# Kernel tuning notes

Measured on AMD Instinct MI355X. Metric: run time of the kernel, lower is better.

Reference implementation:

```python
import jax, jax.numpy as jnp
import numpy as np

EPS = 1e-5
NEG = -1e9

def _ln(x, g, b):
    m = x.mean(-1, keepdims=True)
    v = ((x - m) ** 2).mean(-1, keepdims=True)
    return (x - m) / jnp.sqrt(v + EPS) * g + b

def setup_inputs() -> dict:
    key = jax.random.key(0)
    ks = jax.random.split(key, 32)
    B, N, D, F, L = 2, 512, 128, 512, 3
    s = 0.05
    rn = lambda k, sh, sc=s: jax.random.normal(k, sh, jnp.float32) * sc
    inp = {
        'rel_matrix': rn(ks[0], (B, N, N, 2), 1.0),
        'pre_w': rn(ks[1], (2, D)), 'pre_b': rn(ks[2], (D,)),
        'proj_w': rn(ks[3], (2 * D, D)), 'proj_b': rn(ks[4], (D,)),
        'out_w1': rn(ks[5], (D, D)),
        'bn_g': 1.0 + rn(ks[6], (D,)), 'bn_b': rn(ks[7], (D,)),
        'bn_m': rn(ks[8], (D,)),
        'bn_v': 0.5 + jax.random.uniform(ks[9], (D,), jnp.float32),
        'out_w2': rn(ks[10], (D, D)), 'out_b2': rn(ks[11], (D,)),
        'pe': rn(ks[12], (128, D)),
        'wq': rn(ks[13], (L, D, D)), 'bq': rn(ks[14], (L, D)),
        'wk': rn(ks[15], (L, D, D)), 'bk': rn(ks[16], (L, D)),
        'wv': rn(ks[17], (L, D, D)), 'bv': rn(ks[18], (L, D)),
        'wo': rn(ks[19], (L, D, D)), 'bo': rn(ks[20], (L, D)),
        'ln1g': jnp.ones((L, D), jnp.float32), 'ln1b': jnp.zeros((L, D), jnp.float32),
        'ln2g': jnp.ones((L, D), jnp.float32), 'ln2b': jnp.zeros((L, D), jnp.float32),
        'fw1': rn(ks[21], (L, D, F)), 'fb1': rn(ks[22], (L, F)),
        'fw2': rn(ks[23], (L, F, D)), 'fb2': rn(ks[24], (L, D)),
        'mask': jax.random.randint(ks[25], (B, N), 0, 2) > 0,
        'agent_id': jax.random.randint(ks[26], (B, N), 0, 128, dtype=jnp.int32),
    }
    return inp

def reference(rel_matrix, pre_w, pre_b, proj_w, proj_b, out_w1, bn_g, bn_b, bn_m, bn_v,
              out_w2, out_b2, pe, wq, bq, wk, bk, wv, bv, wo, bo,
              ln1g, ln1b, ln2g, ln2b, fw1, fb1, fw2, fb2, mask, agent_id):
    # --- pairwise relation chain (the headroom target) ---
    # symmetric pairwise validity mask (B,N,N)
    pm = (mask[:, None, :] & mask[:, :, None]).astype(rel_matrix.dtype)
    count = jnp.maximum(pm.sum(axis=2), 1.0)  # (B,N) valid-partner counts
    x = rel_matrix @ pre_w + pre_b            # (B,N,N,D) pre_proj Linear(2->128)
    pooled = jnp.einsum('bijd,bij->bid', x, pm) / count[..., None]  # masked mean over j
    x = jnp.concatenate([x, jnp.broadcast_to(pooled[:, :, None, :], x.shape)], axis=-1)
    x = x @ proj_w + proj_b                   # Linear(256->128)
    x = jnp.einsum('bijd,bij->bid', x, pm) / count[..., None]       # masked mean over j
    # out MLP: Linear(no bias) + BatchNorm1d(eval) + ReLU + Linear
    h = x @ out_w1
    h = (h - bn_m) / jnp.sqrt(bn_v + EPS) * bn_g + bn_b
    x = jax.nn.relu(h) @ out_w2 + out_b2
    x = x + pe[agent_id]                      # agent positional embedding
    # --- 3 post-norm single-head transformer layers (eval, dropout off) ---
    kbias = jnp.where(mask, 0.0, NEG)[:, None, :]  # key padding bias (B,1,N)
    scale = 1.0 / jnp.sqrt(jnp.asarray(x.shape[-1], x.dtype))
    for l in range(3):
        q = x @ wq[l] + bq[l]
        k = x @ wk[l] + bk[l]
        v = x @ wv[l] + bv[l]
        a = jax.nn.softmax(jnp.einsum('bid,bjd->bij', q, k) * scale + kbias, axis=-1)
        att = jnp.einsum('bij,bjd->bid', a, v) @ wo[l] + bo[l]
        x = _ln(x + att, ln1g[l], ln1b[l])
        ff = jax.nn.relu(x @ fw1[l] + fb1[l]) @ fw2[l] + fb2[l]
        x = _ln(x + ff, ln2g[l], ln2b[l])
    return x
```

## Files before the change

kernel.cpp:

```cpp
#include <hip/hip_runtime.h>
#include <hip/hip_bf16.h>

typedef unsigned short u16;
typedef unsigned int u32;
typedef unsigned char u8;
typedef __attribute__((ext_vector_type(8))) short bf16x8;
typedef __attribute__((ext_vector_type(4))) float f32x4;

#define DEV __device__ __forceinline__

DEV float bf2f(u16 u) { union { u32 i; float f; } c; c.i = ((u32)u) << 16; return c.f; }
DEV u16 f2bf(float f) {
  union { float f; u32 i; } c; c.f = f;
  u32 r = c.i + 0x7FFFu + ((c.i >> 16) & 1u);
  return (u16)(r >> 16);
}
DEV u32 pk2(float lo, float hi) { return (u32)f2bf(lo) | ((u32)f2bf(hi) << 16); }
DEV float rdsrc(const void* p, int e, int isb) {
  return isb ? bf2f(((const u16*)p)[e]) : ((const float*)p)[e];
}
DEV bf16x8 as_bf(uint4 v) { union { uint4 u; bf16x8 h; } c; c.u = v; return c.h; }

static constexpr int B = 2, N = 512, D = 128, F = 512;
static constexpr int NROW = B * N;
static constexpr float EPS = 1e-5f;
static constexpr float NEG = -1e9f;
static constexpr float SCALE = 0.08838834764831845f;

#define OFF_PRE_W   0
#define OFF_PRE_B   256
#define OFF_PROJ_B  33152
#define OFF_BN_G    49664
#define OFF_BN_B    49792
#define OFF_BN_M    49920
#define OFF_BN_V    50048
#define OFF_OUT_B2  66560
#define OFF_PE      66688
#define OFF_BQ      132224
#define OFF_BK      181760
#define OFF_BV      231296
#define OFF_BO      280832
#define OFF_LN1G    281216
#define OFF_LN1B    281600
#define OFF_LN2G    281984
#define OFF_LN2B    282368
#define OFF_FB1     479360
#define OFF_FB2     677504
#define W_TOTAL     677888

static constexpr int PB_PROJ = 0;
static constexpr int PB_OW1  = 8192;
static constexpr int PB_OW2  = 16384;
static constexpr int PB_L0   = 24576;
static constexpr int PB_LSTR = 98304;
static constexpr int PB_WO   = 24576;
static constexpr int PB_FW1  = 32768;
static constexpr int PB_FW2  = 65536;
static constexpr int PTOT    = 79872;

struct NEnt { const void* s; int off, n; };
struct PEnt { const void* s1; const void* s2; int o1, o2, dst, lgn, cum; };
struct PrepArgs { NEnt nrm[19]; PEnt pk[21]; };

template<int KT>
DEV f32x4 mmaKo(const uint4* __restrict__ aPk, const uint4* __restrict__ Bp,
                int ncol, int col, int lane, int kt0) {
  f32x4 acc = {0.f, 0.f, 0.f, 0.f};
  const int sub = lane >> 4;
  #pragma unroll
  for (int kt = 0; kt < KT; ++kt) {
    const int e8 = (kt0 + kt) * 4 + sub;
    acc = __builtin_amdgcn_mfma_f32_16x16x32_bf16(
        as_bf(aPk[e8 * 16 + (lane & 15)]),
        as_bf(Bp[(size_t)e8 * ncol + col]),
        acc, 0, 0, 0);
  }
  return acc;
}

DEV void packA(const float* __restrict__ src, int ld, int K,
               uint4* __restrict__ aPk, int t, int nthr) {
  const int n = (K >> 3) * 4;
  for (int i = t; i < n; i += nthr) {
    const int e8 = i >> 2, r = i & 3;
    const float* s = src + r * ld + e8 * 8;
    uint4 w;
    w.x = pk2(s[0], s[1]); w.y = pk2(s[2], s[3]);
    w.z = pk2(s[4], s[5]); w.w = pk2(s[6], s[7]);
    aPk[e8 * 16 + r] = w;
  }
}

__global__ __launch_bounds__(256) void k_prep(PrepArgs pa,
    const void* __restrict__ bnv, const void* __restrict__ maskp,
    int* __restrict__ flags, int* __restrict__ mbuf,
    float* __restrict__ W, u32* __restrict__ Wb)
{
  const int t = threadIdx.x, bid = blockIdx.x;
  __shared__ int s_nb, s_m4, s_m2;
  if (t == 0) { s_nb = 0; s_m4 = 0; s_m2 = 0; }
  __syncthreads();
  if (t < 64) {
    const u32 w = ((const u32*)bnv)[t];
    if (((w >> 8) & 0xFFu) != 0x3Fu || ((w >> 24) & 0xFFu) != 0x3Fu)
      atomicOr(&s_nb, 1);
  }
  __syncthreads();
  const int isb = s_nb ? 0 : 1;

  if (bid < 16) {
    for (int ten = 0; ten < 19; ++ten) {
      const NEnt E = pa.nrm[ten];
      for (int e = bid * 256 + t; e < E.n; e += 16 * 256)
        W[E.off + e] = rdsrc(E.s, e, isb);
    }
  } else if (bid < 511) {
    for (int g = (bid - 16) * 256 + t; g < PTOT; g += 495 * 256) {
      int ei = 0;
      #pragma unroll
      for (int k = 1; k < 21; ++k) if (g >= pa.pk[k].cum) ei = k;
      const PEnt E = pa.pk[ei];
      const int li = g - E.cum;
      const int e8 = li >> E.lgn, c = li & ((1 << E.lgn) - 1);
      float f[8];
      #pragma unroll
      for (int i = 0; i < 8; ++i) {
        const int si = ((e8 * 8 + i) << E.lgn) + c;
        f[i] = rdsrc(E.s1, E.o1 + si, isb);
        if (E.s2) f[i] += rdsrc(E.s2, E.o2 + si, isb);
      }
      uint4 w;
      w.x = pk2(f[0], f[1]); w.y = pk2(f[2], f[3]);
      w.z = pk2(f[4], f[5]); w.w = pk2(f[6], f[7]);
      ((uint4*)(Wb + E.dst))[li] = w;
    }
  } else {
    {
      const u32 w = ((const u32*)maskp)[t];
      if (!(w == 0u || w == 1u || w == 0x3F800000u)) atomicOr(&s_m4, 1);
      if (!(w == 0u || w == 1u || w == 0x10000u || w == 0x10001u ||
            w == 0x3F80u || w == 0x3F800000u || w == 0x3F803F80u)) atomicOr(&s_m2, 1);
    }
    __syncthreads();
    const int mode = (!s_m4) ? 4 : ((!s_m2) ? 2 : 1);
    if (t == 0) { flags[0] = isb; flags[1] = mode; }
    #pragma unroll
    for (int k = 0; k < 4; ++k) {
      const int e = k * 256 + t;
      int v;
      if (mode == 4)      v = (((const u32*)maskp)[e] != 0u);
      else if (mode == 2) v = (((const u16*)maskp)[e] != 0);
      else                v = (((const u8*)maskp)[e]  != 0);
      mbuf[e] = v;
    }
  }
}

__global__ __launch_bounds__(512) void k_relq(
    const void* __restrict__ relv, const float* __restrict__ W,
    const u32* __restrict__ Wb,
    const int* __restrict__ flags, const int* __restrict__ mbuf,
    const int* __restrict__ agent_id, float* __restrict__ xbuf,
    float* __restrict__ qb, u32* __restrict__ kbT, u32* __restrict__ vbT)
{
  const int t = threadIdx.x;
  const int row0 = blockIdx.x * 4;
  const int b = row0 >> 9;
  const int wid = t >> 6;
  const int lane = t & 63;

  __shared__ float pl[4][D], zl[4][D], rl[4][D], os[4][D];
  __shared__ float pA[4][D], pB[4][D];
  __shared__ uint4 aPk[1024];
  __shared__ float wred[8][9];
  __shared__ float sT0[4], sT1[4], sMt;

  float s0[4] = {0, 0, 0, 0}, s1[4] = {0, 0, 0, 0}, cnt;
  {
    const int j = t;
    const float m = (float)mbuf[b * N + j];
    cnt = m;
    if (flags[0]) {
      const u32* rel2 = (const u32*)relv;
      #pragma unroll
      for (int r = 0; r < 4; ++r) {
        const u32 u = rel2[(size_t)(row0 + r) * N + j];
        s0[r] += m * bf2f((u16)(u & 0xFFFFu));
        s1[r] += m * bf2f((u16)(u >> 16));
      }
    } else {
      const float2* relf = (const float2*)relv;
      #pragma unroll
      for (int r = 0; r < 4; ++r) {
        const float2 u = relf[(size_t)(row0 + r) * N + j];
        s0[r] += m * u.x; s1[r] += m * u.y;
      }
    }
  }
  {
    const uint4 z = {0u, 0u, 0u, 0u};
    aPk[t] = z; aPk[t + 512] = z;
  }
  #pragma unroll
  for (int o = 32; o > 0; o >>= 1) {
    #pragma unroll
    for (int r = 0; r < 4; ++r) {
      s0[r] += __shfl_xor(s0[r], o, 64);
      s1[r] += __shfl_xor(s1[r], o, 64);
    }
    cnt += __shfl_xor(cnt, o, 64);
  }
  if ((t & 63) == 0) {
    #pragma unroll
    for (int r = 0; r < 4; ++r) { wred[wid][r] = s0[r]; wred[wid][4 + r] = s1[r]; }
    wred[wid][8] = cnt;
  }
  __syncthreads();
  if (t < 4) {
    float a0 = 0, a1 = 0;
    #pragma unroll
    for (int w = 0; w < 8; ++w) { a0 += wred[w][t]; a1 += wred[w][4 + t]; }
    sT0[t] = a0; sT1[t] = a1;
  }
  if (t == 8) {
    float c = 0;
    #pragma unroll
    for (int w = 0; w < 8; ++w) c += wred[w][8];
    sMt = c;
  }
  __syncthreads();

  {
    const int r = t >> 7, c = t & 127;
    const int mi = mbuf[row0 + r];
    pl[r][c] = mi ? (sT0[r] * W[OFF_PRE_W + c] + sT1[r] * W[OFF_PRE_W + D + c]) / sMt
                    + W[OFF_PRE_B + c]
                  : 0.f;
  }
  __syncthreads();

  packA(&pl[0][0], D, D, aPk, t, 512);
  __syncthreads();
  {
    const int col = wid * 16 + (lane & 15);
    f32x4 acc = mmaKo<4>(aPk, (const uint4*)(Wb + PB_PROJ), 128, col, lane, 0);
    if (lane < 16) {
      #pragma unroll
      for (int g = 0; g < 4; ++g) pA[g][col] = acc[g];
    }
  }
  __syncthreads();
  {
    const int r = t >> 7, d = t & 127;
    zl[r][d] = mbuf[row0 + r] ? pA[r][d] + W[OFF_PROJ_B + d] : 0.f;
  }
  __syncthreads();

  packA(&zl[0][0], D, D, aPk, t, 512);
  __syncthreads();
  {
    const int col = wid * 16 + (lane & 15);
    f32x4 acc = mmaKo<4>(aPk, (const uint4*)(Wb + PB_OW1), 128, col, lane, 0);
    if (lane < 16) {
      #pragma unroll
      for (int g = 0; g < 4; ++g) pA[g][col] = acc[g];
    }
  }
  __syncthreads();
  {
    const int r = t >> 7, d = t & 127;
    const float hb = (pA[r][d] - W[OFF_BN_M + d]) * __frsqrt_rn(W[OFF_BN_V + d] + EPS)
                     * W[OFF_BN_G + d] + W[OFF_BN_B + d];
    rl[r][d] = fmaxf(hb, 0.f);
  }
  __syncthreads();

  packA(&rl[0][0], D, D, aPk, t, 512);
  __syncthreads();
  {
    const int col = wid * 16 + (lane & 15);
    f32x4 acc = mmaKo<4>(aPk, (const uint4*)(Wb + PB_OW2), 128, col, lane, 0);
    if (lane < 16) {
      #pragma unroll
      for (int g = 0; g < 4; ++g) pA[g][col] = acc[g];
    }
  }
  __syncthreads();
  {
    const int r = t >> 7, d = t & 127;
    const int aid = agent_id[row0 + r];
    const float x0 = pA[r][d] + W[OFF_OUT_B2 + d] + W[OFF_PE + aid * D + d];
    os[r][d] = x0;
    xbuf[(size_t)(row0 + r) * D + d] = x0;
  }
  __syncthreads();

  packA(&os[0][0], D, D, aPk, t, 512);
  __syncthreads();
  {
    const int col = wid * 16 + (lane & 15);
    #pragma unroll
    for (int m = 0; m < 3; ++m) {
      f32x4 acc = mmaKo<4>(aPk, (const uint4*)(Wb + PB_L0 + m * 8192), 128, col, lane, 0);
      if (lane < 16) {
        const float bb = W[(m == 0 ? OFF_BQ : m == 1 ? OFF_BK : OFF_BV) + col];
        if (m == 0) {
          #pragma unroll
          for (int g = 0; g < 4; ++g) qb[(size_t)(row0 + g) * D + col] = acc[g] + bb;
        } else if (m == 1) {
          #pragma unroll
          for (int g = 0; g < 4; ++g) pA[g][col] = acc[g] + bb;
        } else {
          #pragma unroll
          for (int g = 0; g < 4; ++g) pB[g][col] = acc[g] + bb;
        }
      }
    }
  }
  __syncthreads();
  if (t < 64) {
    const int r = t >> 4, e8 = t & 15;
    const float* ks = pA[r];
    uint4 w;
    w.x = pk2(ks[8 * e8 + 0], ks[8 * e8 + 1]);
    w.y = pk2(ks[8 * e8 + 2], ks[8 * e8 + 3]);
    w.z = pk2(ks[8 * e8 + 4], ks[8 * e8 + 5]);
    w.w = pk2(ks[8 * e8 + 6], ks[8 * e8 + 7]);
    ((uint4*)kbT)[((size_t)b * 16 + e8) * 512 + (row0 & 511) + r] = w;
  }
  if (t < 128) {
    const int i0 = row0 & 511, j8 = i0 >> 3, h = (i0 >> 2) & 1;
    uint2 w;
    w.x = pk2(pB[0][t], pB[1][t]);
    w.y = pk2(pB[2][t], pB[3][t]);
    *(uint2*)(vbT + (((size_t)b * 64 + j8) * 128 + t) * 4 + 2 * h) = w;
  }
}

__global__ __launch_bounds__(1024) void k_layer(
    const float* __restrict__ qin, const u32* __restrict__ kinT, const u32* __restrict__ vinT,
    const float* __restrict__ W, const u32* __restrict__ Wb, const int l, const int last,
    float* __restrict__ qout, u32* __restrict__ koutT, u32* __restrict__ voutT,
    const int* __restrict__ mbuf, float* __restrict__ xbuf, float* __restrict__ outp)
{
  const int t = threadIdx.x;
  const int row0 = blockIdx.x * 4;
  const int b = row0 >> 9;
  const int wid = t >> 6;
  const int lane = t & 63;
  const int w8 = wid & 7, half = wid >> 3;

  const uint4* WOp = (const uint4*)(Wb + PB_L0 + l * PB_LSTR + PB_WO);
  const uint4* W1p = (const uint4*)(Wb + PB_L0 + l * PB_LSTR + PB_FW1);
  const uint4* W2p = (const uint4*)(Wb + PB_L0 + l * PB_LSTR + PB_FW2);
  const float* bo  = W + OFF_BO  + l * D;
  const float* g1  = W + OFF_LN1G + l * D;
  const float* b1  = W + OFF_LN1B + l * D;
  const float* fb1 = W + OFF_FB1 + l * F;
  const float* fb2 = W + OFF_FB2 + l * D;
  const float* g2  = W + OFF_LN2G + l * D;
  const float* b2v = W + OFF_LN2B + l * D;

  __shared__ float qs[4][D];
  __shared__ float bufA[4][512];
  __shared__ float os[4][D];
  __shared__ float xs[4][D];
  __shared__ float pA[4][D], pB[4][D];
  __shared__ uint4 aPk[1024];
  __shared__ float den[4];

  if (t < 512) {
    const int r = t >> 7, d = t & 127;
    qs[r][d] = qin[(size_t)(row0 + r) * D + d] * SCALE;
  }
  {
    const uint4 z = {0u, 0u, 0u, 0u};
    aPk[t & 1023] = z;
  }
  __syncthreads();

  packA(&qs[0][0], D, D, aPk, t, 1024);
  __syncthreads();
  {
    const uint4* Kp = (const uint4*)kinT + (size_t)b * 16 * 512;
    #pragma unroll
    for (int ii = 0; ii < 2; ++ii) {
      const int col = (wid + 16 * ii) * 16 + (lane & 15);
      f32x4 acc = mmaKo<4>(aPk, Kp, 512, col, lane, 0);
      if (lane < 16) {
        const float bias = mbuf[b * N + col] ? 0.f : NEG;
        #pragma unroll
        for (int g = 0; g < 4; ++g) bufA[g][col] = acc[g] + bias;
      }
    }
  }
  __syncthreads();

  if (wid < 4) {
    const int r = wid;
    float pv[8];
    float mx = -1e30f;
    #pragma unroll
    for (int k = 0; k < 8; ++k) { pv[k] = bufA[r][lane + 64 * k]; mx = fmaxf(mx, pv[k]); }
    #pragma unroll
    for (int o = 32; o > 0; o >>= 1) mx = fmaxf(mx, __shfl_xor(mx, o, 64));
    float sum = 0.f;
    #pragma unroll
    for (int k = 0; k < 8; ++k) { pv[k] = __expf(pv[k] - mx); sum += pv[k]; }
    #pragma unroll
    for (int o = 32; o > 0; o >>= 1) sum += __shfl_xor(sum, o, 64);
    #pragma unroll
    for (int k = 0; k < 8; ++k) bufA[r][lane + 64 * k] = pv[k];
    if (lane == 0) den[r] = sum;
  }
  __syncthreads();

  packA(&bufA[0][0], N, N, aPk, t, 1024);
  __syncthreads();
  {
    const int col = w8 * 16 + (lane & 15);
    const uint4* Vp = (const uint4*)vinT + (size_t)b * 64 * 128;
    f32x4 acc = mmaKo<8>(aPk, Vp, 128, col, lane, half * 8);
    if (lane < 16) {
      float* dst = half ? &pB[0][0] : &pA[0][0];
      #pragma unroll
      for (int g = 0; g < 4; ++g) dst[g * D + col] = acc[g];
    }
  }
  __syncthreads();
  if (t < 512) {
    const int r = t >> 7, d = t & 127;
    os[r][d] = (pA[r][d] + pB[r][d]) / den[r];
  }
  __syncthreads();

  packA(&os[0][0], D, D, aPk, t, 1024);
  __syncthreads();
  {
    const int col = w8 * 16 + (lane & 15);
    f32x4 acc = mmaKo<2>(aPk, WOp, 128, col, lane, half * 2);
    if (lane < 16) {
      float* dst = half ? &pB[0][0] : &pA[0][0];
      #pragma unroll
      for (int g = 0; g < 4; ++g) dst[g * D + col] = acc[g];
    }
  }
  __syncthreads();

  if (wid < 4) {
    const int r = wid;
    float tv[2];
    #pragma unroll
    for (int k = 0; k < 2; ++k) {
      const int d = lane + 64 * k;
      tv[k] = pA[r][d] + pB[r][d] + bo[d] + xbuf[(size_t)(row0 + r) * D + d];
    }
    float s = tv[0] + tv[1], sq = tv[0] * tv[0] + tv[1] * tv[1];
    #pragma unroll
    for (int o = 32; o > 0; o >>= 1) { s += __shfl_xor(s, o, 64); sq += __shfl_xor(sq, o, 64); }
    const float mean = s * (1.f / 128.f);
    const float var  = sq * (1.f / 128.f) - mean * mean;
    const float rstd = __frsqrt_rn(var + EPS);
    #pragma unroll
    for (int k = 0; k < 2; ++k) {
      const int d = lane + 64 * k;
      xs[r][d] = (tv[k] - mean) * rstd * g1[d] + b1[d];
    }
  }
  __syncthreads();

  packA(&xs[0][0], D, D, aPk, t, 1024);
  __syncthreads();
  {
    #pragma unroll
    for (int ii = 0; ii < 2; ++ii) {
      const int col = (wid + 16 * ii) * 16 + (lane & 15);
      f32x4 acc = mmaKo<4>(aPk, W1p, 512, col, lane, 0);
      if (lane < 16) {
        const float bb = fb1[col];
        #pragma unroll
        for (int g = 0; g < 4; ++g) bufA[g][col] = fmaxf(acc[g] + bb, 0.f);
      }
    }
  }
  __syncthreads();

  packA(&bufA[0][0], F, F, aPk, t, 1024);
  __syncthreads();
  {
    const int col = w8 * 16 + (lane & 15);
    f32x4 acc = mmaKo<8>(aPk, W2p, 128, col, lane, half * 8);
    if (lane < 16) {
      float* dst = half ? &pB[0][0] : &pA[0][0];
      #pragma unroll
      for (int g = 0; g < 4; ++g) dst[g * D + col] = acc[g];
    }
  }
  __syncthreads();

  if (wid < 4) {
    const int r = wid;
    float tv[2];
    #pragma unroll
    for (int k = 0; k < 2; ++k) {
      const int d = lane + 64 * k;
      tv[k] = pA[r][d] + pB[r][d] + fb2[d] + xs[r][d];
    }
    float s = tv[0] + tv[1], sq = tv[0] * tv[0] + tv[1] * tv[1];
    #pragma unroll
    for (int o = 32; o > 0; o >>= 1) { s += __shfl_xor(s, o, 64); sq += __shfl_xor(sq, o, 64); }
    const float mean = s * (1.f / 128.f);
    const float var  = sq * (1.f / 128.f) - mean * mean;
    const float rstd = __frsqrt_rn(var + EPS);
    #pragma unroll
    for (int k = 0; k < 2; ++k) {
      const int d = lane + 64 * k;
      const float xn = (tv[k] - mean) * rstd * g2[d] + b2v[d];
      os[r][d] = xn;
      xbuf[(size_t)(row0 + r) * D + d] = xn;
      if (last) outp[(size_t)(row0 + r) * D + d] = xn;
    }
  }
  __syncthreads();

  if (!last) {
    packA(&os[0][0], D, D, aPk, t, 1024);
    __syncthreads();
    #pragma unroll
    for (int it = 0; it < 2; ++it) {
      const int task = wid + 16 * it;
      if (task < 24) {
        const int m = task >> 3, c8 = task & 7;
        const int col = c8 * 16 + (lane & 15);
        const uint4* Bp = (const uint4*)(Wb + PB_L0 + (l + 1) * PB_LSTR + m * 8192);
        f32x4 acc = mmaKo<4>(aPk, Bp, 128, col, lane, 0);
        if (lane < 16) {
          const float bb = W[(m == 0 ? OFF_BQ : m == 1 ? OFF_BK : OFF_BV) + (l + 1) * D + col];
          if (m == 0) {
            #pragma unroll
            for (int g = 0; g < 4; ++g) qout[(size_t)(row0 + g) * D + col] = acc[g] + bb;
          } else if (m == 1) {
            #pragma unroll
            for (int g = 0; g < 4; ++g) pA[g][col] = acc[g] + bb;
          } else {
            #pragma unroll
            for (int g = 0; g < 4; ++g) pB[g][col] = acc[g] + bb;
          }
        }
      }
    }
    __syncthreads();
    if (t < 64) {
      const int r = t >> 4, e8 = t & 15;
      const float* ks = pA[r];
      uint4 w;
      w.x = pk2(ks[8 * e8 + 0], ks[8 * e8 + 1]);
      w.y = pk2(ks[8 * e8 + 2], ks[8 * e8 + 3]);
      w.z = pk2(ks[8 * e8 + 4], ks[8 * e8 + 5]);
      w.w = pk2(ks[8 * e8 + 6], ks[8 * e8 + 7]);
      ((uint4*)koutT)[((size_t)b * 16 + e8) * 512 + (row0 & 511) + r] = w;
    }
    if (t < 128) {
      const int i0 = row0 & 511, j8 = i0 >> 3, h = (i0 >> 2) & 1;
      uint2 w;
      w.x = pk2(pB[0][t], pB[1][t]);
      w.y = pk2(pB[2][t], pB[3][t]);
      *(uint2*)(voutT + (((size_t)b * 64 + j8) * 128 + t) * 4 + 2 * h) = w;
    }
  }
}

extern "C" void kernel_launch(void* const* d_in, const int* in_sizes, int n_in,
                              void* d_out, int out_size, void* d_ws, size_t ws_size,
                              hipStream_t stream) {
  int*   flags = (int*)d_ws;
  int*   mbuf  = flags + 16;
  float* xbuf  = (float*)d_ws + 1040;
  float* q0    = xbuf + NROW * D;
  float* q1    = q0 + NROW * D;
  u32*   kT0   = (u32*)(q1 + NROW * D);
  u32*   kT1   = kT0 + 65536;
  u32*   vT0   = kT1 + 65536;
  u32*   vT1   = vT0 + 65536;
  float* W     = (float*)(vT1 + 65536);
  u32*   Wb    = (u32*)(W + W_TOTAL);

  PrepArgs pa;
  {
    const NEnt nrm[19] = {
      {d_in[1],  OFF_PRE_W,  256}, {d_in[2],  OFF_PRE_B, 128},
      {d_in[4],  OFF_PROJ_B, 128},
      {d_in[6],  OFF_BN_G,   128}, {d_in[7],  OFF_BN_B,  128},
      {d_in[8],  OFF_BN_M,   128}, {d_in[9],  OFF_BN_V,  128},
      {d_in[11], OFF_OUT_B2, 128}, {d_in[12], OFF_PE,  16384},
      {d_in[14], OFF_BQ,     384}, {d_in[16], OFF_BK,    384},
      {d_in[18], OFF_BV,     384}, {d_in[20], OFF_BO,    384},
      {d_in[21], OFF_LN1G,   384}, {d_in[22], OFF_LN1B,  384},
      {d_in[23], OFF_LN2G,   384}, {d_in[24], OFF_LN2B,  384},
      {d_in[26], OFF_FB1,   1536}, {d_in[28], OFF_FB2,   384}};
    for (int i = 0; i < 19; ++i) pa.nrm[i] = nrm[i];

    pa.pk[0] = {d_in[3], d_in[3], 0, 16384, PB_PROJ, 7, 0};
    pa.pk[1] = {d_in[5],  nullptr, 0, 0, PB_OW1, 7, 2048};
    pa.pk[2] = {d_in[10], nullptr, 0, 0, PB_OW2, 7, 4096};
    for (int l = 0; l < 3; ++l) {
      const int lb = PB_L0 + l * PB_LSTR;
      const int cl = 6144 + l * 24576;
      pa.pk[3 + 6 * l + 0] = {d_in[13], nullptr, l * 16384, 0, lb,          7, cl};
      pa.pk[3 + 6 * l + 1] = {d_in[15], nullptr, l * 16384, 0, lb + 8192,   7, cl + 2048};
      pa.pk[3 + 6 * l + 2] = {d_in[17], nullptr, l * 16384, 0, lb + 16384,  7, cl + 4096};
      pa.pk[3 + 6 * l + 3] = {d_in[19], nullptr, l * 16384, 0, lb + PB_WO,  7, cl + 6144};
      pa.pk[3 + 6 * l + 4] = {d_in[25], nullptr, l * 65536, 0, lb + PB_FW1, 9, cl + 8192};
      pa.pk[3 + 6 * l + 5] = {d_in[27], nullptr, l * 65536, 0, lb + PB_FW2, 7, cl + 16384};
    }
  }
  const int* agent_id = (const int*)d_in[30];

  k_prep<<<512, 256, 0, stream>>>(pa, d_in[9], d_in[29], flags, mbuf, W, Wb);
  k_relq<<<NROW / 4, 512, 0, stream>>>(d_in[0], W, Wb, flags, mbuf, agent_id, xbuf,
                                       q0, kT0, vT0);

  float* qs_[2] = {q0, q1};
  u32*   ks_[2] = {kT0, kT1};
  u32*   vs_[2] = {vT0, vT1};
  for (int l = 0; l < 3; ++l) {
    const int cur = l & 1, nxt = cur ^ 1;
    const int last = (l == 2);
    k_layer<<<NROW / 4, 1024, 0, stream>>>(
        qs_[cur], ks_[cur], vs_[cur],
        W, Wb, l, last,
        qs_[nxt], ks_[nxt], vs_[nxt],
        mbuf, xbuf, last ? (float*)d_out : (float*)nullptr);
  }
}
```

Measured before the change: 67.80 us.

## Pack MFMA operands directly from registers and drop staging barriers

Epilogues of each MFMA stage now convert results to bf16 pairs with a lane shuffle and write straight into the packed A-operand layout. This removes the intermediate fp32 shared buffers and the separate packA passes. Two ping-pong packed buffers replace the single one, which eliminates roughly one __syncthreads per stage. K and V transposed outputs are written directly from MFMA results rather than through shared staging. The cost is extra shuffles and a scattered 32-bit LDS and global store pattern.

```diff
diff --git a/kernel.cpp b/kernel.cpp
--- a/kernel.cpp
+++ b/kernel.cpp
@@ -78,16 +78,22 @@
   return acc;
 }
 
-DEV void packA(const float* __restrict__ src, int ld, int K,
-               uint4* __restrict__ aPk, int t, int nthr) {
-  const int n = (K >> 3) * 4;
-  for (int i = t; i < n; i += nthr) {
-    const int e8 = i >> 2, r = i & 3;
-    const float* s = src + r * ld + e8 * 8;
-    uint4 w;
-    w.x = pk2(s[0], s[1]); w.y = pk2(s[2], s[3]);
-    w.z = pk2(s[4], s[5]); w.w = pk2(s[6], s[7]);
-    aPk[e8 * 16 + r] = w;
+DEV void packRD(u32* aPkU, int r, int d, float v) {
+  const float p = __shfl_xor(v, 1, 64);
+  if (!(d & 1))
+    aPkU[(((d >> 3) * 16 + r) << 2) + ((d >> 1) & 3)] = pk2(v, p);
+}
+
+DEV void packP16(u32* aPkU, int colbase, int lane, f32x4 v) {
+  f32x4 p;
+  #pragma unroll
+  for (int g = 0; g < 4; ++g) p[g] = __shfl_xor(v[g], 1, 64);
+  if (!(lane & 1)) {
+    const int c = colbase + lane;
+    const int e8 = c >> 3, slot = (c >> 1) & 3;
+    #pragma unroll
+    for (int g = 0; g < 4; ++g)
+      aPkU[((e8 * 16 + g) << 2) + slot] = pk2(v[g], p[g]);
   }
 }
 
@@ -169,11 +175,12 @@
   const int wid = t >> 6;
   const int lane = t & 63;
 
-  __shared__ float pl[4][D], zl[4][D], rl[4][D], os[4][D];
-  __shared__ float pA[4][D], pB[4][D];
-  __shared__ uint4 aPk[1024];
+  __shared__ uint4 aPk[2][256];
   __shared__ float wred[8][9];
   __shared__ float sT0[4], sT1[4], sMt;
+
+  u32* a0 = (u32*)&aPk[0][0];
+  u32* a1 = (u32*)&aPk[1][0];
 
   float s0[4] = {0, 0, 0, 0}, s1[4] = {0, 0, 0, 0}, cnt;
   {
@@ -197,9 +204,9 @@
       }
     }
   }
-  {
+  if ((t & 15) >= 4) {
     const uint4 z = {0u, 0u, 0u, 0u};
-    aPk[t] = z; aPk[t + 512] = z;
+    aPk[t >> 8][t & 255] = z;
   }
   #pragma unroll
   for (int o = 32; o > 0; o >>= 1) {
@@ -217,10 +224,10 @@
   }
   __syncthreads();
   if (t < 4) {
-    float a0 = 0, a1 = 0;
-    #pragma unroll
-    for (int w = 0; w < 8; ++w) { a0 += wred[w][t]; a1 += wred[w][4 + t]; }
-    sT0[t] = a0; sT1[t] = a1;
+    float a0v = 0, a1v = 0;
+    #pragma unroll
+    for (int w = 0; w < 8; ++w) { a0v += wred[w][t]; a1v += wred[w][4 + t]; }
+    sT0[t] = a0v; sT1[t] = a1v;
   }
   if (t == 8) {
     float c = 0;
@@ -233,107 +240,89 @@
   {
     const int r = t >> 7, c = t & 127;
     const int mi = mbuf[row0 + r];
-    pl[r][c] = mi ? (sT0[r] * W[OFF_PRE_W + c] + sT1[r] * W[OFF_PRE_W + D + c]) / sMt
-                    + W[OFF_PRE_B + c]
-                  : 0.f;
-  }
-  __syncthreads();
-
-  packA(&pl[0][0], D, D, aPk, t, 512);
-  __syncthreads();
+    const float v = mi ? (sT0[r] * W[OFF_PRE_W + c] + sT1[r] * W[OFF_PRE_W + D + c]) / sMt
+                         + W[OFF_PRE_B + c]
+                       : 0.f;
+    packRD(a0, r, c, v);
+  }
+  __syncthreads();
+
   {
     const int col = wid * 16 + (lane & 15);
-    f32x4 acc = mmaKo<4>(aPk, (const uint4*)(Wb + PB_PROJ), 128, col, lane, 0);
+    f32x4 acc = mmaKo<4>(&aPk[0][0], (const uint4*)(Wb + PB_PROJ), 128, col, lane, 0);
     if (lane < 16) {
-      #pragma unroll
-      for (int g = 0; g < 4; ++g) pA[g][col] = acc[g];
-    }
-  }
-  __syncthreads();
-  {
-    const int r = t >> 7, d = t & 127;
-    zl[r][d] = mbuf[row0 + r] ? pA[r][d] + W[OFF_PROJ_B + d] : 0.f;
-  }
-  __syncthreads();
-
-  packA(&zl[0][0], D, D, aPk, t, 512);
-  __syncthreads();
+      const float pb = W[OFF_PROJ_B + col];
+      f32x4 v;
+      #pragma unroll
+      for (int g = 0; g < 4; ++g) v[g] = mbuf[row0 + g] ? acc[g] + pb : 0.f;
+      packP16(a1, wid * 16, lane, v);
+    }
+  }
+  __syncthreads();
+
   {
     const int col = wid * 16 + (lane & 15);
-    f32x4 acc = mmaKo<4>(aPk, (const uint4*)(Wb + PB_OW1), 128, col, lane, 0);
+    f32x4 acc = mmaKo<4>(&aPk[1][0], (const uint4*)(Wb + PB_OW1), 128, col, lane, 0);
     if (lane < 16) {
-      #pragma unroll
-      for (int g = 0; g < 4; ++g) pA[g][col] = acc[g];
-    }
-  }
-  __syncthreads();
-  {
-    const int r = t >> 7, d = t & 127;
-    const float hb = (pA[r][d] - W[OFF_BN_M + d]) * __frsqrt_rn(W[OFF_BN_V + d] + EPS)
-                     * W[OFF_BN_G + d] + W[OFF_BN_B + d];
-    rl[r][d] = fmaxf(hb, 0.f);
-  }
-  __syncthreads();
-
-  packA(&rl[0][0], D, D, aPk, t, 512);
-  __syncthreads();
+      const float bnm = W[OFF_BN_M + col];
+      const float rs  = __frsqrt_rn(W[OFF_BN_V + col] + EPS);
+      const float bg  = W[OFF_BN_G + col], bb = W[OFF_BN_B + col];
+      f32x4 v;
+      #pragma unroll
+      for (int g = 0; g < 4; ++g) v[g] = fmaxf((acc[g] - bnm) * rs * bg + bb, 0.f);
+      packP16(a0, wid * 16, lane, v);
+    }
+  }
+  __syncthreads();
+
   {
     const int col = wid * 16 + (lane & 15);
-    f32x4 acc = mmaKo<4>(aPk, (const uint4*)(Wb + PB_OW2), 128, col, lane, 0);
+    f32x4 acc = mmaKo<4>(&aPk[0][0], (const uint4*)(Wb + PB_OW2), 128, col, lane, 0);
     if (lane < 16) {
-      #pragma unroll
-      for (int g = 0; g < 4; ++g) pA[g][col] = acc[g];
-    }
-  }
-  __syncthreads();
-  {
-    const int r = t >> 7, d = t & 127;
-    const int aid = agent_id[row0 + r];
-    const float x0 = pA[r][d] + W[OFF_OUT_B2 + d] + W[OFF_PE + aid * D + d];
-    os[r][d] = x0;
-    xbuf[(size_t)(row0 + r) * D + d] = x0;
-  }
-  __syncthreads();
-
-  packA(&os[0][0], D, D, aPk, t, 512);
-  __syncthreads();
+      const float ob = W[OFF_OUT_B2 + col];
+      f32x4 v;
+      #pragma unroll
+      for (int g = 0; g < 4; ++g) {
+        const int aid = agent_id[row0 + g];
+        v[g] = acc[g] + ob + W[OFF_PE + aid * D + col];
+        xbuf[(size_t)(row0 + g) * D + col] = v[g];
+      }
+      packP16(a1, wid * 16, lane, v);
+    }
+  }
+  __syncthreads();
+
   {
     const int col = wid * 16 + (lane & 15);
+    const int i0 = row0 & 511;
     #pragma unroll
     for (int m = 0; m < 3; ++m) {
-      f32x4 acc = mmaKo<4>(aPk, (const uint4*)(Wb + PB_L0 + m * 8192), 128, col, lane, 0);
+      f32x4 acc = mmaKo<4>(&aPk[1][0], (const uint4*)(Wb + PB_L0 + m * 8192), 128, col, lane, 0);
       if (lane < 16) {
         const float bb = W[(m == 0 ? OFF_BQ : m == 1 ? OFF_BK : OFF_BV) + col];
+        f32x4 v;
+        #pragma unroll
+        for (int g = 0; g < 4; ++g) v[g] = acc[g] + bb;
         if (m == 0) {
           #pragma unroll
-          for (int g = 0; g < 4; ++g) qb[(size_t)(row0 + g) * D + col] = acc[g] + bb;
+          for (int g = 0; g < 4; ++g) qb[(size_t)(row0 + g) * D + col] = v[g];
         } else if (m == 1) {
+          f32x4 p;
           #pragma unroll
-          for (int g = 0; g < 4; ++g) pA[g][col] = acc[g] + bb;
+          for (int g = 0; g < 4; ++g) p[g] = __shfl_xor(v[g], 1, 64);
+          if (!(lane & 1)) {
+            const int e8 = col >> 3, slot = (col >> 1) & 3;
+            #pragma unroll
+            for (int g = 0; g < 4; ++g)
+              ((u32*)kbT)[(((size_t)b * 16 + e8) * 512 + i0 + g) * 4 + slot] = pk2(v[g], p[g]);
+          }
         } else {
-          #pragma unroll
-          for (int g = 0; g < 4; ++g) pB[g][col] = acc[g] + bb;
+          uint2 w;
+          w.x = pk2(v[0], v[1]); w.y = pk2(v[2], v[3]);
+          *(uint2*)(vbT + (((size_t)b * 64 + (i0 >> 3)) * 128 + col) * 4 + 2 * ((i0 >> 2) & 1)) = w;
         }
       }
     }
-  }
-  __syncthreads();
-  if (t < 64) {
-    const int r = t >> 4, e8 = t & 15;
-    const float* ks = pA[r];
-    uint4 w;
-    w.x = pk2(ks[8 * e8 + 0], ks[8 * e8 + 1]);
-    w.y = pk2(ks[8 * e8 + 2], ks[8 * e8 + 3]);
-    w.z = pk2(ks[8 * e8 + 4], ks[8 * e8 + 5]);
-    w.w = pk2(ks[8 * e8 + 6], ks[8 * e8 + 7]);
-    ((uint4*)kbT)[((size_t)b * 16 + e8) * 512 + (row0 & 511) + r] = w;
-  }
-  if (t < 128) {
-    const int i0 = row0 & 511, j8 = i0 >> 3, h = (i0 >> 2) & 1;
-    uint2 w;
-    w.x = pk2(pB[0][t], pB[1][t]);
-    w.y = pk2(pB[2][t], pB[3][t]);
-    *(uint2*)(vbT + (((size_t)b * 64 + j8) * 128 + t) * 4 + 2 * h) = w;
   }
 }
 
@@ -361,32 +350,32 @@
   const float* g2  = W + OFF_LN2G + l * D;
   const float* b2v = W + OFF_LN2B + l * D;
 
-  __shared__ float qs[4][D];
   __shared__ float bufA[4][512];
-  __shared__ float os[4][D];
   __shared__ float xs[4][D];
   __shared__ float pA[4][D], pB[4][D];
-  __shared__ uint4 aPk[1024];
+  __shared__ uint4 aPk[2][1024];
   __shared__ float den[4];
 
+  u32* a0 = (u32*)&aPk[0][0];
+  u32* a1 = (u32*)&aPk[1][0];
+
+  for (int i = t; i < 2048; i += 1024)
+    if ((i & 15) >= 4) {
+      const uint4 z = {0u, 0u, 0u, 0u};
+      aPk[i >> 10][i & 1023] = z;
+    }
   if (t < 512) {
     const int r = t >> 7, d = t & 127;
-    qs[r][d] = qin[(size_t)(row0 + r) * D + d] * SCALE;
-  }
-  {
-    const uint4 z = {0u, 0u, 0u, 0u};
-    aPk[t & 1023] = z;
-  }
-  __syncthreads();
-
-  packA(&qs[0][0], D, D, aPk, t, 1024);
-  __syncthreads();
+    packRD(a0, r, d, qin[(size_t)(row0 + r) * D + d] * SCALE);
+  }
+  __syncthreads();
+
   {
     const uint4* Kp = (const uint4*)kinT + (size_t)b * 16 * 512;
     #pragma unroll
     for (int ii = 0; ii < 2; ++ii) {
       const int col = (wid + 16 * ii) * 16 + (lane & 15);
-      f32x4 acc = mmaKo<4>(aPk, Kp, 512, col, lane, 0);
+      f32x4 acc = mmaKo<4>(&aPk[0][0], Kp, 512, col, lane, 0);
       if (lane < 16) {
         const float bias = mbuf[b * N + col] ? 0.f : NEG;
         #pragma unroll
@@ -410,17 +399,21 @@
     #pragma unroll
     for (int o = 32; o > 0; o >>= 1) sum += __shfl_xor(sum, o, 64);
     #pragma unroll
-    for (int k = 0; k < 8; ++k) bufA[r][lane + 64 * k] = pv[k];
+    for (int k = 0; k < 8; ++k) {
+      const float pp = __shfl_xor(pv[k], 1, 64);
+      if (!(lane & 1)) {
+        const int c = lane + 64 * k;
+        a1[(((c >> 3) * 16 + r) << 2) + ((c >> 1) & 3)] = pk2(pv[k], pp);
+      }
+    }
     if (lane == 0) den[r] = sum;
   }
   __syncthreads();
 
-  packA(&bufA[0][0], N, N, aPk, t, 1024);
-  __syncthreads();
   {
     const int col = w8 * 16 + (lane & 15);
     const uint4* Vp = (const uint4*)vinT + (size_t)b * 64 * 128;
-    f32x4 acc = mmaKo<8>(aPk, Vp, 128, col, lane, half * 8);
+    f32x4 acc = mmaKo<8>(&aPk[1][0], Vp, 128, col, lane, half * 8);
     if (lane < 16) {
       float* dst = half ? &pB[0][0] : &pA[0][0];
       #pragma unroll
@@ -428,17 +421,16 @@
     }
   }
   __syncthreads();
+
   if (t < 512) {
     const int r = t >> 7, d = t & 127;
-    os[r][d] = (pA[r][d] + pB[r][d]) / den[r];
-  }
-  __syncthreads();
-
-  packA(&os[0][0], D, D, aPk, t, 1024);
-  __syncthreads();
+    packRD(a0, r, d, (pA[r][d] + pB[r][d]) / den[r]);
+  }
+  __syncthreads();
+
   {
     const int col = w8 * 16 + (lane & 15);
-    f32x4 acc = mmaKo<2>(aPk, WOp, 128, col, lane, half * 2);
+    f32x4 acc = mmaKo<2>(&aPk[0][0], WOp, 128, col, lane, half * 2);
     if (lane < 16) {
       float* dst = half ? &pB[0][0] : &pA[0][0];
       #pragma unroll
@@ -464,32 +456,35 @@
     #pragma unroll
     for (int k = 0; k < 2; ++k) {
       const int d = lane + 64 * k;
-      xs[r][d] = (tv[k] - mean) * rstd * g1[d] + b1[d];
-    }
-  }
-  __syncthreads();
-
-  packA(&xs[0][0], D, D, aPk, t, 1024);
-  __syncthreads();
+      const float xn = (tv[k] - mean) * rstd * g1[d] + b1[d];
+      xs[r][d] = xn;
+      const float pp = __shfl_xor(xn, 1, 64);
+      if (!(lane & 1))
+        a1[(((d >> 3) * 16 + r) << 2) + ((d >> 1) & 3)] = pk2(xn, pp);
+    }
+  }
+  __syncthreads();
+
   {
     #pragma unroll
     for (int ii = 0; ii < 2; ++ii) {
-      const int col = (wid + 16 * ii) * 16 + (lane & 15);
-      f32x4 acc = mmaKo<4>(aPk, W1p, 512, col, lane, 0);
+      const int colbase = (wid + 16 * ii) * 16;
+      const int col = colbase + (lane & 15);
+      f32x4 acc = mmaKo<4>(&aPk[1][0], W1p, 512, col, lane, 0);
       if (lane < 16) {
         const float bb = fb1[col];
+        f32x4 v;
         #pragma unroll
-        for (int g = 0; g < 4; ++g) bufA[g][col] = fmaxf(acc[g] + bb, 0.f);
-      }
-    }
-  }
-  __syncthreads();
-
-  packA(&bufA[0][0], F, F, aPk, t, 1024);
-  __syncthreads();
+        for (int g = 0; g < 4; ++g) v[g] = fmaxf(acc[g] + bb, 0.f);
+        packP16(a0, colbase, lane, v);
+      }
+    }
+  }
+  __syncthreads();
+
   {
     const int col = w8 * 16 + (lane & 15);
-    f32x4 acc = mmaKo<8>(aPk, W2p, 128, col, lane, half * 8);
+    f32x4 acc = mmaKo<8>(&aPk[0][0], W2p, 128, col, lane, half * 8);
     if (lane < 16) {
       float* dst = half ? &pB[0][0] : &pA[0][0];
       #pragma unroll
@@ -516,16 +511,17 @@
     for (int k = 0; k < 2; ++k) {
       const int d = lane + 64 * k;
       const float xn = (tv[k] - mean) * rstd * g2[d] + b2v[d];
-      os[r][d] = xn;
       xbuf[(size_t)(row0 + r) * D + d] = xn;
       if (last) outp[(size_t)(row0 + r) * D + d] = xn;
-    }
-  }
-  __syncthreads();
+      const float pp = __shfl_xor(xn, 1, 64);
+      if (!last && !(lane & 1))
+        a1[(((d >> 3) * 16 + r) << 2) + ((d >> 1) & 3)] = pk2(xn, pp);
+    }
+  }
 
   if (!last) {
-    packA(&os[0][0], D, D, aPk, t, 1024);
     __syncthreads();
+    const int i0 = row0 & 511;
     #pragma unroll
     for (int it = 0; it < 2; ++it) {
       const int task = wid + 16 * it;
@@ -533,39 +529,32 @@
         const int m = task >> 3, c8 = task & 7;
         const int col = c8 * 16 + (lane & 15);
         const uint4* Bp = (const uint4*)(Wb + PB_L0 + (l + 1) * PB_LSTR + m * 8192);
-        f32x4 acc = mmaKo<4>(aPk, Bp, 128, col, lane, 0);
+        f32x4 acc = mmaKo<4>(&aPk[1][0], Bp, 128, col, lane, 0);
         if (lane < 16) {
           const float bb = W[(m == 0 ? OFF_BQ : m == 1 ? OFF_BK : OFF_BV) + (l + 1) * D + col];
+          f32x4 v;
+          #pragma unroll
+          for (int g = 0; g < 4; ++g) v[g] = acc[g] + bb;
           if (m == 0) {
             #pragma unroll
-            for (int g = 0; g < 4; ++g) qout[(size_t)(row0 + g) * D + col] = acc[g] + bb;
+            for (int g = 0; g < 4; ++g) qout[(size_t)(row0 + g) * D + col] = v[g];
           } else if (m == 1) {
+            f32x4 p;
             #pragma unroll
-            for (int g = 0; g < 4; ++g) pA[g][col] = acc[g] + bb;
+            for (int g = 0; g < 4; ++g) p[g] = __shfl_xor(v[g], 1, 64);
+            if (!(lane & 1)) {
+              const int e8 = col >> 3, slot = (col >> 1) & 3;
+              #pragma unroll
+              for (int g = 0; g < 4; ++g)
+                ((u32*)koutT)[(((size_t)b * 16 + e8) * 512 + i0 + g) * 4 + slot] = pk2(v[g], p[g]);
+            }
           } else {
-            #pragma unroll
-            for (int g = 0; g < 4; ++g) pB[g][col] = acc[g] + bb;
+            uint2 w;
+            w.x = pk2(v[0], v[1]); w.y = pk2(v[2], v[3]);
+            *(uint2*)(voutT + (((size_t)b * 64 + (i0 >> 3)) * 128 + col) * 4 + 2 * ((i0 >> 2) & 1)) = w;
           }
         }
       }
-    }
-    __syncthreads();
-    if (t < 64) {
-      const int r = t >> 4, e8 = t & 15;
-      const float* ks = pA[r];
-      uint4 w;
-      w.x = pk2(ks[8 * e8 + 0], ks[8 * e8 + 1]);
-      w.y = pk2(ks[8 * e8 + 2], ks[8 * e8 + 3]);
-      w.z = pk2(ks[8 * e8 + 4], ks[8 * e8 + 5]);
-      w.w = pk2(ks[8 * e8 + 6], ks[8 * e8 + 7]);
-      ((uint4*)koutT)[((size_t)b * 16 + e8) * 512 + (row0 & 511) + r] = w;
-    }
-    if (t < 128) {
-      const int i0 = row0 & 511, j8 = i0 >> 3, h = (i0 >> 2) & 1;
-      uint2 w;
-      w.x = pk2(pB[0][t], pB[1][t]);
-      w.y = pk2(pB[2][t], pB[3][t]);
-      *(uint2*)(voutT + (((size_t)b * 64 + j8) * 128 + t) * 4 + 2 * h) = w;
     }
   }
 }
```

New measurement: 66.63 us. About the same (-1.7%).
